# Optimization experiments

Measured on AMD Instinct MI355X. Metric: run time of the kernel, lower is better.

Reference implementation:

```python
import jax, jax.numpy as jnp
import numpy as np

DIM = 1024
N_HEADS = 16
HEAD_DIM = DIM // N_HEADS


def setup_inputs() -> dict:
    key = jax.random.key(0)
    ks = jax.random.split(key, 5)
    B, L = 2, 2048
    q = jax.random.normal(ks[0], (B, L, DIM), dtype=jnp.float32)
    # nn.Linear weights: shape [out_features, in_features], applied as x @ W.T
    scale = 1.0 / np.sqrt(DIM)
    Wq = jax.random.normal(ks[1], (DIM, DIM), dtype=jnp.float32) * scale
    Wk = jax.random.normal(ks[2], (DIM, DIM), dtype=jnp.float32) * scale
    Wv = jax.random.normal(ks[3], (DIM, DIM), dtype=jnp.float32) * scale
    Wo = jax.random.normal(ks[4], (DIM, DIM), dtype=jnp.float32) * scale
    return {"q": q, "Wq": Wq, "Wk": Wk, "Wv": Wv, "Wo": Wo}


def reference(q, Wq, Wk, Wv, Wo):
    B, L, _ = q.shape
    kv = q  # self-attention (kv=None path)
    # projections: x @ W.T, then split heads: b l (h d) -> b h l d
    def split_heads(x):
        return x.reshape(B, L, N_HEADS, HEAD_DIM).transpose(0, 2, 1, 3)
    qh = split_heads(q @ Wq.T)
    kh = split_heads(kv @ Wk.T)
    vh = split_heads(kv @ Wv.T)
    # scaled dot-product attention; scale = sqrt(head_dim)
    scores = jnp.einsum('bhid,bhjd->bhij', qh, kh) / jnp.sqrt(
        jnp.asarray(HEAD_DIM, dtype=qh.dtype))
    attn = jax.nn.softmax(scores, axis=-1)
    out = jnp.einsum('bhij,bhjd->bhid', attn, vh)
    # b h l d -> b l (h d)
    out = out.transpose(0, 2, 1, 3).reshape(B, L, DIM)
    return out @ Wo.T
```

## Files before the change

kernel.cpp:

```cpp
#include <hip/hip_runtime.h>


#define DIMN 1024
#define NH 16
#define HD 64
#define BB 2
#define LL 2048

typedef float f32x4 __attribute__((ext_vector_type(4)));
typedef short s16x8 __attribute__((ext_vector_type(8)));

#define QSCALE 0.18033688011112042f

static __device__ __forceinline__ unsigned short f2bf(float f) {
  unsigned u = __float_as_uint(f);
  u += 0x7fffu + ((u >> 16) & 1u);
  return (unsigned short)(u >> 16);
}
static __device__ __forceinline__ unsigned packbf2(float lo, float hi) {
  return (unsigned)f2bf(lo) | ((unsigned)f2bf(hi) << 16);
}
static __device__ __forceinline__ float xexp2(float x) {
#if __has_builtin(__builtin_amdgcn_exp2f)
  return __builtin_amdgcn_exp2f(x);
#else
  return exp2f(x);
#endif
}
static __device__ __forceinline__ s16x8 cvt8(float4 a, float4 b) {
  s16x8 r;
  r[0] = (short)f2bf(a.x); r[1] = (short)f2bf(a.y);
  r[2] = (short)f2bf(a.z); r[3] = (short)f2bf(a.w);
  r[4] = (short)f2bf(b.x); r[5] = (short)f2bf(b.y);
  r[6] = (short)f2bf(b.z); r[7] = (short)f2bf(b.w);
  return r;
}
static __device__ __forceinline__ void gld16(const unsigned short* g,
                                             unsigned short* l) {
#if __has_builtin(__builtin_amdgcn_global_load_lds)
  __builtin_amdgcn_global_load_lds(
      (const __attribute__((address_space(1))) void*)g,
      (__attribute__((address_space(3))) void*)l, 16, 0, 0);
#else
  ((uint4*)l)[threadIdx.x & 63] = ((const uint4*)g)[0];
#endif
}


__global__ __launch_bounds__(256) void cvt_all(
    const float* __restrict__ X, const float* __restrict__ Wq,
    const float* __restrict__ Wk, const float* __restrict__ Wv,
    const float* __restrict__ Wo, unsigned short* __restrict__ out) {
  const int blk = blockIdx.x;
  const float* src;
  unsigned short* dst;
  size_t off;
  if (blk < 2048) {
    src = X; dst = out; off = (size_t)blk * 2048;
  } else {
    int s = (blk - 2048) >> 9;
    src = (s == 0) ? Wq : (s == 1) ? Wk : (s == 2) ? Wv : Wo;
    dst = out + ((size_t)1 << 22) + (size_t)s * (1u << 20);
    off = (size_t)((blk - 2048) & 511) * 2048;
  }
  size_t i = off + (size_t)threadIdx.x * 8;
  float4 v0 = *(const float4*)(src + i);
  float4 v1 = *(const float4*)(src + i + 4);
  uint4 o;
  o.x = packbf2(v0.x, v0.y); o.y = packbf2(v0.z, v0.w);
  o.z = packbf2(v1.x, v1.y); o.w = packbf2(v1.z, v1.w);
  *(uint4*)(dst + i) = o;
}

__global__ __launch_bounds__(256) void gemm_qkv(
    const unsigned short* __restrict__ Xb, const unsigned short* __restrict__ Wb,
    unsigned short* __restrict__ Qb, unsigned short* __restrict__ Kb,
    unsigned short* __restrict__ VT) {
  __shared__ __align__(16) unsigned short Al[128 * 32];
  __shared__ __align__(16) unsigned short Bl[128 * 32];
  const int m0 = blockIdx.x * 128;
  const int n0g = blockIdx.y * 128;
  const int sel = n0g >> 10;
  const int tid = threadIdx.x;
  const int w = tid >> 6, lane = tid & 63;
  const int c = lane & 15, quad = lane >> 4;
  const int wm = (w & 1) * 64, wn = (w >> 1) * 64;

  f32x4 zero = {0.f, 0.f, 0.f, 0.f};
  f32x4 acc[4][4];
#pragma unroll
  for (int i = 0; i < 4; ++i)
#pragma unroll
    for (int j = 0; j < 4; ++j) acc[i][j] = zero;

  const int srow = w * 32 + (lane >> 2);
  const int scol = (lane & 3) * 8;
  const unsigned short* gA = Xb + (size_t)(m0 + srow) * DIMN + scol;
  const unsigned short* gB = Wb + (size_t)(n0g + srow) * DIMN + scol;
  unsigned short* lA0 = Al + (w * 32) * 32;
  unsigned short* lA1 = Al + (w * 32 + 16) * 32;
  unsigned short* lB0 = Bl + (w * 32) * 32;
  unsigned short* lB1 = Bl + (w * 32 + 16) * 32;

  for (int k0 = 0; k0 < DIMN; k0 += 32) {
    __syncthreads();
    gld16(gA + k0, lA0);
    gld16(gA + k0 + 16 * DIMN, lA1);
    gld16(gB + k0, lB0);
    gld16(gB + k0 + 16 * DIMN, lB1);
    __syncthreads();
    s16x8 a[4], b[4];
#pragma unroll
    for (int i = 0; i < 4; ++i)
      a[i] = *(const s16x8*)&Al[(wm + i * 16 + c) * 32 + quad * 8];
#pragma unroll
    for (int j = 0; j < 4; ++j)
      b[j] = *(const s16x8*)&Bl[(wn + j * 16 + c) * 32 + quad * 8];
    if (sel != 2) {
#pragma unroll
      for (int i = 0; i < 4; ++i)
#pragma unroll
        for (int j = 0; j < 4; ++j)
          acc[i][j] = __builtin_amdgcn_mfma_f32_16x16x32_bf16(a[i], b[j], acc[i][j], 0, 0, 0);
    } else {
#pragma unroll
      for (int i = 0; i < 4; ++i)
#pragma unroll
        for (int j = 0; j < 4; ++j)
          acc[i][j] = __builtin_amdgcn_mfma_f32_16x16x32_bf16(b[j], a[i], acc[i][j], 0, 0, 0);
    }
  }

  const int n0 = n0g & 1023;
  if (sel != 2) {
    unsigned short* Out = (sel == 0) ? Qb : Kb;
    const float scale = (sel == 0) ? QSCALE : 1.0f;
#pragma unroll
    for (int i = 0; i < 4; ++i)
#pragma unroll
      for (int j = 0; j < 4; ++j)
#pragma unroll
        for (int r = 0; r < 4; ++r) {
          int row = m0 + wm + i * 16 + quad * 4 + r;
          int col = n0 + wn + j * 16 + c;
          Out[(((size_t)(row >> 11) * NH + (col >> 6)) * LL + (row & 2047)) * HD + (col & 63)] =
              f2bf(acc[i][j][r] * scale);
        }
  } else {
#pragma unroll
    for (int i = 0; i < 4; ++i) {
      const int p64 = (i >> 1) * 32 + (i & 1);
#pragma unroll
      for (int j = 0; j < 4; ++j)
#pragma unroll
        for (int r = 0; r < 4; ++r) {
          int n = n0 + wn + j * 16 + quad * 4 + r;
          int m = m0 + wm + p64 + 2 * c;
          VT[(((size_t)(m >> 11) * NH + (n >> 6)) * HD + (n & 63)) * LL + (m & 2047)] =
              f2bf(acc[i][j][r]);
        }
    }
  }
}

__global__ __launch_bounds__(256) void gemm_o(
    const unsigned short* __restrict__ A, const unsigned short* __restrict__ Wob,
    float* __restrict__ Out) {
  __shared__ __align__(16) unsigned short Al[128 * 32];
  __shared__ __align__(16) unsigned short Bl[64 * 32];
  const int m0 = blockIdx.x * 128;
  const int n0 = blockIdx.y * 64;
  const int tid = threadIdx.x;
  const int w = tid >> 6, lane = tid & 63;
  const int c = lane & 15, quad = lane >> 4;
  const int wm = (w & 1) * 64, wn = (w >> 1) * 32;

  f32x4 zero = {0.f, 0.f, 0.f, 0.f};
  f32x4 acc[4][2];
#pragma unroll
  for (int i = 0; i < 4; ++i)
#pragma unroll
    for (int j = 0; j < 2; ++j) acc[i][j] = zero;

  const int srow = w * 32 + (lane >> 2);
  const int brow = w * 16 + (lane >> 2);
  const int scol = (lane & 3) * 8;
  const unsigned short* gA = A + (size_t)(m0 + srow) * DIMN + scol;
  const unsigned short* gB = Wob + (size_t)(n0 + brow) * DIMN + scol;
  unsigned short* lA0 = Al + (w * 32) * 32;
  unsigned short* lA1 = Al + (w * 32 + 16) * 32;
  unsigned short* lB0 = Bl + (w * 16) * 32;

  for (int k0 = 0; k0 < DIMN; k0 += 32) {
    __syncthreads();
    gld16(gA + k0, lA0);
    gld16(gA + k0 + 16 * DIMN, lA1);
    gld16(gB + k0, lB0);
    __syncthreads();
    s16x8 a[4], b[2];
#pragma unroll
    for (int i = 0; i < 4; ++i)
      a[i] = *(const s16x8*)&Al[(wm + i * 16 + c) * 32 + quad * 8];
#pragma unroll
    for (int j = 0; j < 2; ++j)
      b[j] = *(const s16x8*)&Bl[(wn + j * 16 + c) * 32 + quad * 8];
#pragma unroll
    for (int i = 0; i < 4; ++i)
#pragma unroll
      for (int j = 0; j < 2; ++j)
        acc[i][j] = __builtin_amdgcn_mfma_f32_16x16x32_bf16(a[i], b[j], acc[i][j], 0, 0, 0);
  }

#pragma unroll
  for (int i = 0; i < 4; ++i)
#pragma unroll
    for (int j = 0; j < 2; ++j)
#pragma unroll
      for (int r = 0; r < 4; ++r)
        Out[(size_t)(m0 + wm + i * 16 + quad * 4 + r) * DIMN + n0 + wn + j * 16 + c] =
            acc[i][j][r];
}

__global__ __launch_bounds__(256) void attn4(
    const unsigned short* __restrict__ Qb, const unsigned short* __restrict__ Kb,
    const unsigned short* __restrict__ VT, unsigned short* __restrict__ AO) {
  __shared__ __align__(16) unsigned short Kl[128 * 64];
  __shared__ __align__(16) unsigned short Vtl[64 * 128];
  __shared__ __align__(16) unsigned short Pl[4][32][72];

  const int bh = blockIdx.y;
  const int tid = threadIdx.x;
  const int w = tid >> 6, lane = tid & 63;
  const int c = lane & 15, quad = lane >> 4;
  const int q0 = blockIdx.x * 128 + w * 32;

  const unsigned short* Qh = Qb + (size_t)bh * LL * HD;
  const unsigned short* Kh = Kb + (size_t)bh * LL * HD;
  const unsigned short* Vh = VT + (size_t)bh * HD * LL;

  s16x8 qf[2][2];
#pragma unroll
  for (int m = 0; m < 2; ++m)
#pragma unroll
    for (int f = 0; f < 2; ++f)
      qf[m][f] = *(const s16x8*)(Qh + (size_t)(q0 + m * 16 + c) * HD + f * 32 + quad * 8);

  f32x4 zero = {0.f, 0.f, 0.f, 0.f};
  f32x4 o[2][4];
  float lsum[2][4];
#pragma unroll
  for (int m = 0; m < 2; ++m)
#pragma unroll
    for (int r = 0; r < 4; ++r) lsum[m][r] = 0.f;
#pragma unroll
  for (int m = 0; m < 2; ++m)
#pragma unroll
    for (int dc = 0; dc < 4; ++dc) o[m][dc] = zero;

  const int l8 = lane >> 3, p8 = lane & 7;
  const unsigned short* gK = Kh + (size_t)(w * 8 + l8) * HD + ((p8 ^ l8) * 8);
  unsigned short* lK = (unsigned short*)Kl + (w * 8) * 64;
  const int l16 = lane >> 4, p16 = lane & 15;
  const int vrow = w * 4 + l16;
  const unsigned short* gV = Vh + (size_t)vrow * LL + ((p16 ^ vrow) * 8);
  unsigned short* lV = (unsigned short*)Vtl + (w * 4) * 128;

  const int kpa = (quad ^ (c & 7)) * 8;
  const int kpb = ((quad + 4) ^ (c & 7)) * 8;

  for (int k0 = 0; k0 < LL; k0 += 128) {
    __syncthreads();
#pragma unroll
    for (int s = 0; s < 4; ++s)
      gld16(gK + (size_t)(k0 + s * 32) * HD, lK + s * 32 * 64);
#pragma unroll
    for (int s = 0; s < 4; ++s)
      gld16(gV + (size_t)(s * 16) * LL + k0, lV + s * 16 * 128);
    __syncthreads();

#pragma unroll
    for (int g = 0; g < 2; ++g) {
      f32x4 s[2][4];
#pragma unroll
      for (int t4 = 0; t4 < 4; ++t4) {
        const int t = g * 4 + t4;
        s16x8 kfa = *(const s16x8*)&Kl[(t * 16 + c) * 64 + kpa];
        s16x8 kfb = *(const s16x8*)&Kl[(t * 16 + c) * 64 + kpb];
#pragma unroll
        for (int m = 0; m < 2; ++m) {
          s[m][t4] = __builtin_amdgcn_mfma_f32_16x16x32_bf16(qf[m][0], kfa, zero, 0, 0, 0);
          s[m][t4] = __builtin_amdgcn_mfma_f32_16x16x32_bf16(qf[m][1], kfb, s[m][t4], 0, 0, 0);
        }
      }
#pragma unroll
      for (int m = 0; m < 2; ++m)
#pragma unroll
        for (int r = 0; r < 4; ++r) {
          float p0 = xexp2(s[m][0][r]);
          float p1 = xexp2(s[m][1][r]);
          float p2 = xexp2(s[m][2][r]);
          float p3 = xexp2(s[m][3][r]);
          lsum[m][r] += (p0 + p1) + (p2 + p3);
          unsigned pk01 = __builtin_amdgcn_perm(__float_as_uint(p1), __float_as_uint(p0), 0x07060302u);
          unsigned pk23 = __builtin_amdgcn_perm(__float_as_uint(p3), __float_as_uint(p2), 0x07060302u);
          int row = m * 16 + quad * 4 + r;
          *(unsigned*)&Pl[w][row][2 * c] = pk01;
          *(unsigned*)&Pl[w][row][32 + 2 * c] = pk23;
        }
      asm volatile("s_waitcnt lgkmcnt(0)" ::: "memory");

#pragma unroll
      for (int kh = 0; kh < 2; ++kh) {
        const int kk = g * 2 + kh;
        s16x8 pf0 = *(const s16x8*)&Pl[w][c][kh * 32 + quad * 8];
        s16x8 pf1 = *(const s16x8*)&Pl[w][16 + c][kh * 32 + quad * 8];
#pragma unroll
        for (int dc = 0; dc < 4; ++dc) {
          s16x8 vf = *(const s16x8*)&Vtl[(dc * 16 + c) * 128 + (((kk * 4 + quad) ^ c) * 8)];
          o[0][dc] = __builtin_amdgcn_mfma_f32_16x16x32_bf16(pf0, vf, o[0][dc], 0, 0, 0);
          o[1][dc] = __builtin_amdgcn_mfma_f32_16x16x32_bf16(pf1, vf, o[1][dc], 0, 0, 0);
        }
      }
    }
  }

  const int bi = bh >> 4, h = bh & 15;
#pragma unroll
  for (int m = 0; m < 2; ++m)
#pragma unroll
    for (int r = 0; r < 4; ++r) {
      float l = lsum[m][r];
      l += __shfl_xor(l, 1);
      l += __shfl_xor(l, 2);
      l += __shfl_xor(l, 4);
      l += __shfl_xor(l, 8);
      float inv = 1.0f / l;
      int li = q0 + m * 16 + quad * 4 + r;
#pragma unroll
      for (int dc = 0; dc < 4; ++dc)
        AO[((size_t)bi * LL + li) * DIMN + h * HD + dc * 16 + c] = f2bf(o[m][dc][r] * inv);
    }
}

__global__ __launch_bounds__(64) void qkv_proj_f(
    const float* __restrict__ X, const float* __restrict__ Wq,
    const float* __restrict__ Wk, const float* __restrict__ Wv,
    unsigned short* __restrict__ Qb, unsigned short* __restrict__ Kb,
    unsigned short* __restrict__ VT) {
  const int m0 = blockIdx.x * 64;
  const int n0g = blockIdx.y * 64;
  const int sel = n0g >> 10;
  const int n0 = n0g & 1023;
  const float* W = (sel == 0) ? Wq : (sel == 1) ? Wk : Wv;
  const int lane = threadIdx.x;
  const int c = lane & 15, quad = lane >> 4;

  f32x4 zero = {0.f, 0.f, 0.f, 0.f};
  f32x4 acc[4][4];
#pragma unroll
  for (int i = 0; i < 4; ++i)
#pragma unroll
    for (int j = 0; j < 4; ++j) acc[i][j] = zero;

  const float* ab = X + (size_t)(m0 + c) * DIMN + quad * 8;
  const float* bb = W + (size_t)(n0 + c) * DIMN + quad * 8;

  for (int k0 = 0; k0 < DIMN; k0 += 32) {
    s16x8 a[4], b[4];
#pragma unroll
    for (int i = 0; i < 4; ++i) {
      const float* p = ab + i * 16 * DIMN + k0;
      a[i] = cvt8(*(const float4*)p, *(const float4*)(p + 4));
    }
#pragma unroll
    for (int j = 0; j < 4; ++j) {
      const float* p = bb + j * 16 * DIMN + k0;
      b[j] = cvt8(*(const float4*)p, *(const float4*)(p + 4));
    }
    if (sel != 2) {
#pragma unroll
      for (int i = 0; i < 4; ++i)
#pragma unroll
        for (int j = 0; j < 4; ++j)
          acc[i][j] = __builtin_amdgcn_mfma_f32_16x16x32_bf16(a[i], b[j], acc[i][j], 0, 0, 0);
    } else {
#pragma unroll
      for (int i = 0; i < 4; ++i)
#pragma unroll
        for (int j = 0; j < 4; ++j)
          acc[i][j] = __builtin_amdgcn_mfma_f32_16x16x32_bf16(b[j], a[i], acc[i][j], 0, 0, 0);
    }
  }

  if (sel != 2) {
    unsigned short* Out = (sel == 0) ? Qb : Kb;
    const float scale = (sel == 0) ? QSCALE : 1.0f;
#pragma unroll
    for (int i = 0; i < 4; ++i)
#pragma unroll
      for (int j = 0; j < 4; ++j)
#pragma unroll
        for (int r = 0; r < 4; ++r) {
          int row = m0 + i * 16 + quad * 4 + r;
          int nl = n0 + j * 16 + c;
          int bi = row >> 11, li = row & 2047;
          int h = nl >> 6, d = nl & 63;
          Out[(((size_t)bi * NH + h) * LL + li) * HD + d] = f2bf(acc[i][j][r] * scale);
        }
  } else {
#pragma unroll
    for (int i = 0; i < 4; ++i) {
      const int p64 = (i >> 1) * 32 + (i & 1);
#pragma unroll
      for (int j = 0; j < 4; ++j)
#pragma unroll
        for (int r = 0; r < 4; ++r) {
          int n = n0 + j * 16 + quad * 4 + r;
          int l = m0 + p64 + 2 * c;
          int h = n >> 6, d = n & 63;
          int bi = l >> 11, li = l & 2047;
          VT[(((size_t)bi * NH + h) * HD + d) * LL + li] = f2bf(acc[i][j][r]);
        }
    }
  }
}

__global__ __launch_bounds__(64) void o_proj_f(
    const unsigned short* __restrict__ A, const float* __restrict__ Wo,
    float* __restrict__ Out) {
  const int m0 = blockIdx.x * 64, n0 = blockIdx.y * 64;
  const int lane = threadIdx.x;
  const int c = lane & 15, quad = lane >> 4;

  f32x4 zero = {0.f, 0.f, 0.f, 0.f};
  f32x4 acc[4][4];
#pragma unroll
  for (int i = 0; i < 4; ++i)
#pragma unroll
    for (int j = 0; j < 4; ++j) acc[i][j] = zero;

  const unsigned short* ab = A + (size_t)(m0 + c) * DIMN + quad * 8;
  const float* bb = Wo + (size_t)(n0 + c) * DIMN + quad * 8;

  for (int k0 = 0; k0 < DIMN; k0 += 32) {
    s16x8 a[4], b[4];
#pragma unroll
    for (int i = 0; i < 4; ++i) a[i] = *(const s16x8*)(ab + i * 16 * DIMN + k0);
#pragma unroll
    for (int j = 0; j < 4; ++j) {
      const float* p = bb + j * 16 * DIMN + k0;
      b[j] = cvt8(*(const float4*)p, *(const float4*)(p + 4));
    }
#pragma unroll
    for (int i = 0; i < 4; ++i)
#pragma unroll
      for (int j = 0; j < 4; ++j)
        acc[i][j] = __builtin_amdgcn_mfma_f32_16x16x32_bf16(a[i], b[j], acc[i][j], 0, 0, 0);
  }

#pragma unroll
  for (int i = 0; i < 4; ++i)
#pragma unroll
    for (int j = 0; j < 4; ++j)
#pragma unroll
      for (int r = 0; r < 4; ++r)
        Out[(size_t)(m0 + i * 16 + quad * 4 + r) * DIMN + n0 + j * 16 + c] = acc[i][j][r];
}

extern "C" void kernel_launch(void* const* d_in, const int* in_sizes, int n_in,
                              void* d_out, int out_size, void* d_ws, size_t ws_size,
                              hipStream_t stream) {
  const float* X = (const float*)d_in[0];
  const float* Wq = (const float*)d_in[1];
  const float* Wk = (const float*)d_in[2];
  const float* Wv = (const float*)d_in[3];
  const float* Wo = (const float*)d_in[4];
  float* Out = (float*)d_out;

  const size_t M1 = (size_t)1 << 20;
  unsigned short* ws16 = (unsigned short*)d_ws;

  if (ws_size >= (size_t)48 * 1024 * 1024) {
    unsigned short* Xb = ws16;
    unsigned short* Wb = ws16 + 4 * M1;
    unsigned short* Qb = ws16 + 8 * M1;
    unsigned short* Kb = ws16 + 12 * M1;
    unsigned short* VT = ws16 + 16 * M1;
    unsigned short* AO = ws16 + 20 * M1;
    cvt_all<<<4096, 256, 0, stream>>>(X, Wq, Wk, Wv, Wo, ws16);
    gemm_qkv<<<dim3(32, 24), 256, 0, stream>>>(Xb, Wb, Qb, Kb, VT);
    attn4<<<dim3(LL / 128, BB * NH), 256, 0, stream>>>(Qb, Kb, VT, AO);
    gemm_o<<<dim3(32, 16), 256, 0, stream>>>(AO, Wb + 3 * M1, Out);
  } else {
    unsigned short* Qb = ws16;
    unsigned short* Kb = ws16 + 4 * M1;
    unsigned short* VT = ws16 + 8 * M1;
    unsigned short* AO = ws16 + 12 * M1;
    qkv_proj_f<<<dim3(64, 48), 64, 0, stream>>>(X, Wq, Wk, Wv, Qb, Kb, VT);
    attn4<<<dim3(LL / 128, BB * NH), 256, 0, stream>>>(Qb, Kb, VT, AO);
    o_proj_f<<<dim3(64, 16), 64, 0, stream>>>(AO, Wo, Out);
  }
}
```

Before: 196.9 us.

## Keep softmax probabilities in registers via transposed MFMA and permuted V layout

The attention kernel now computes S^T by swapping the MFMA operands, so each lane holds the probabilities for its own query column. These are packed straight into bf16 A-operands for the PV MFMA, which removes the LDS round trip through the P buffer and its wait. To make this work, the V^T columns are written by the projection kernels in a permuted key order (vpos). K/V tiles are also double-buffered, so the next tile's loads are issued while the current one is computed, leaving one barrier per iteration. Output stores become packed 8-byte writes, and the row-sum reduction shrinks to two shuffles. The cost is double the LDS footprint, which may reduce occupancy.

```diff
diff --git a/kernel.cpp b/kernel.cpp
--- a/kernel.cpp
+++ b/kernel.cpp
@@ -46,6 +46,9 @@
 #endif
 }
 
+static __device__ __forceinline__ int vpos(int s128) {
+  return (s128 & 0x60) | ((s128 & 0x0C) << 1) | ((s128 & 0x10) >> 2) | (s128 & 3);
+}
 
 __global__ __launch_bounds__(256) void cvt_all(
     const float* __restrict__ X, const float* __restrict__ Wq,
@@ -149,16 +152,19 @@
   } else {
 #pragma unroll
     for (int i = 0; i < 4; ++i) {
-      const int p64 = (i >> 1) * 32 + (i & 1);
+      const int pos = vpos(wm + i * 16 + 2 * 0 + 0);
 #pragma unroll
       for (int j = 0; j < 4; ++j)
 #pragma unroll
         for (int r = 0; r < 4; ++r) {
           int n = n0 + wn + j * 16 + quad * 4 + r;
-          int m = m0 + wm + p64 + 2 * c;
-          VT[(((size_t)(m >> 11) * NH + (n >> 6)) * HD + (n & 63)) * LL + (m & 2047)] =
+          int sp = vpos(wm + i * 16 + c);
+          int m = m0 + sp;
+          int bi = (m0 + wm) >> 11;
+          VT[(((size_t)bi * NH + (n >> 6)) * HD + (n & 63)) * LL + (m & 2047)] =
               f2bf(acc[i][j][r]);
         }
+      (void)pos;
     }
   }
 }
@@ -221,12 +227,11 @@
             acc[i][j][r];
 }
 
-__global__ __launch_bounds__(256) void attn4(
+__global__ __launch_bounds__(256) void attn5(
     const unsigned short* __restrict__ Qb, const unsigned short* __restrict__ Kb,
     const unsigned short* __restrict__ VT, unsigned short* __restrict__ AO) {
-  __shared__ __align__(16) unsigned short Kl[128 * 64];
-  __shared__ __align__(16) unsigned short Vtl[64 * 128];
-  __shared__ __align__(16) unsigned short Pl[4][32][72];
+  __shared__ __align__(16) unsigned short Kl[2 * 128 * 64];
+  __shared__ __align__(16) unsigned short Vtl[2 * 64 * 128];
 
   const int bh = blockIdx.y;
   const int tid = threadIdx.x;
@@ -247,11 +252,7 @@
 
   f32x4 zero = {0.f, 0.f, 0.f, 0.f};
   f32x4 o[2][4];
-  float lsum[2][4];
-#pragma unroll
-  for (int m = 0; m < 2; ++m)
-#pragma unroll
-    for (int r = 0; r < 4; ++r) lsum[m][r] = 0.f;
+  float lsum[2] = {0.f, 0.f};
 #pragma unroll
   for (int m = 0; m < 2; ++m)
 #pragma unroll
@@ -259,87 +260,105 @@
 
   const int l8 = lane >> 3, p8 = lane & 7;
   const unsigned short* gK = Kh + (size_t)(w * 8 + l8) * HD + ((p8 ^ l8) * 8);
-  unsigned short* lK = (unsigned short*)Kl + (w * 8) * 64;
   const int l16 = lane >> 4, p16 = lane & 15;
   const int vrow = w * 4 + l16;
   const unsigned short* gV = Vh + (size_t)vrow * LL + ((p16 ^ vrow) * 8);
-  unsigned short* lV = (unsigned short*)Vtl + (w * 4) * 128;
 
   const int kpa = (quad ^ (c & 7)) * 8;
   const int kpb = ((quad + 4) ^ (c & 7)) * 8;
 
-  for (int k0 = 0; k0 < LL; k0 += 128) {
+#define STAGE(buf, k0)                                                        \
+  do {                                                                        \
+    unsigned short* lK_ = Kl + (buf) * (128 * 64) + (w * 8) * 64;             \
+    unsigned short* lV_ = Vtl + (buf) * (64 * 128) + (w * 4) * 128;           \
+    _Pragma("unroll")                                                         \
+    for (int s_ = 0; s_ < 4; ++s_)                                            \
+      gld16(gK + (size_t)((k0) + s_ * 32) * HD, lK_ + s_ * 32 * 64);          \
+    _Pragma("unroll")                                                         \
+    for (int s_ = 0; s_ < 4; ++s_)                                            \
+      gld16(gV + (size_t)(s_ * 16) * LL + (k0), lV_ + s_ * 16 * 128);         \
+  } while (0)
+
+  STAGE(0, 0);
+
+  for (int it = 0; it < LL / 128; ++it) {
     __syncthreads();
-#pragma unroll
-    for (int s = 0; s < 4; ++s)
-      gld16(gK + (size_t)(k0 + s * 32) * HD, lK + s * 32 * 64);
-#pragma unroll
-    for (int s = 0; s < 4; ++s)
-      gld16(gV + (size_t)(s * 16) * LL + k0, lV + s * 16 * 128);
-    __syncthreads();
+    if (it + 1 < LL / 128) STAGE((it + 1) & 1, (it + 1) * 128);
+    const unsigned short* Kt = Kl + (it & 1) * (128 * 64);
+    const unsigned short* Vt = Vtl + (it & 1) * (64 * 128);
 
 #pragma unroll
     for (int g = 0; g < 2; ++g) {
       f32x4 s[2][4];
 #pragma unroll
       for (int t4 = 0; t4 < 4; ++t4) {
-        const int t = g * 4 + t4;
-        s16x8 kfa = *(const s16x8*)&Kl[(t * 16 + c) * 64 + kpa];
-        s16x8 kfb = *(const s16x8*)&Kl[(t * 16 + c) * 64 + kpb];
+        const unsigned short* kr = Kt + ((g * 4 + t4) * 16 + c) * 64;
+        s16x8 kfa = *(const s16x8*)(kr + kpa);
+        s16x8 kfb = *(const s16x8*)(kr + kpb);
 #pragma unroll
         for (int m = 0; m < 2; ++m) {
-          s[m][t4] = __builtin_amdgcn_mfma_f32_16x16x32_bf16(qf[m][0], kfa, zero, 0, 0, 0);
-          s[m][t4] = __builtin_amdgcn_mfma_f32_16x16x32_bf16(qf[m][1], kfb, s[m][t4], 0, 0, 0);
+          s[m][t4] = __builtin_amdgcn_mfma_f32_16x16x32_bf16(kfa, qf[m][0], zero, 0, 0, 0);
+          s[m][t4] = __builtin_amdgcn_mfma_f32_16x16x32_bf16(kfb, qf[m][1], s[m][t4], 0, 0, 0);
         }
       }
-#pragma unroll
-      for (int m = 0; m < 2; ++m)
-#pragma unroll
-        for (int r = 0; r < 4; ++r) {
-          float p0 = xexp2(s[m][0][r]);
-          float p1 = xexp2(s[m][1][r]);
-          float p2 = xexp2(s[m][2][r]);
-          float p3 = xexp2(s[m][3][r]);
-          lsum[m][r] += (p0 + p1) + (p2 + p3);
-          unsigned pk01 = __builtin_amdgcn_perm(__float_as_uint(p1), __float_as_uint(p0), 0x07060302u);
-          unsigned pk23 = __builtin_amdgcn_perm(__float_as_uint(p3), __float_as_uint(p2), 0x07060302u);
-          int row = m * 16 + quad * 4 + r;
-          *(unsigned*)&Pl[w][row][2 * c] = pk01;
-          *(unsigned*)&Pl[w][row][32 + 2 * c] = pk23;
-        }
-      asm volatile("s_waitcnt lgkmcnt(0)" ::: "memory");
-
+      float p[2][4][4];
+#pragma unroll
+      for (int m = 0; m < 2; ++m) {
+        float acc_l = 0.f;
+#pragma unroll
+        for (int t4 = 0; t4 < 4; ++t4)
+#pragma unroll
+          for (int r = 0; r < 4; ++r) {
+            float e = xexp2(s[m][t4][r]);
+            p[m][t4][r] = e;
+            acc_l += e;
+          }
+        lsum[m] += acc_l;
+      }
 #pragma unroll
       for (int kh = 0; kh < 2; ++kh) {
         const int kk = g * 2 + kh;
-        s16x8 pf0 = *(const s16x8*)&Pl[w][c][kh * 32 + quad * 8];
-        s16x8 pf1 = *(const s16x8*)&Pl[w][16 + c][kh * 32 + quad * 8];
+        s16x8 pf[2];
+#pragma unroll
+        for (int m = 0; m < 2; ++m) {
+          unsigned u0 = __builtin_amdgcn_perm(__float_as_uint(p[m][2 * kh][1]),
+                                              __float_as_uint(p[m][2 * kh][0]), 0x07060302u);
+          unsigned u1 = __builtin_amdgcn_perm(__float_as_uint(p[m][2 * kh][3]),
+                                              __float_as_uint(p[m][2 * kh][2]), 0x07060302u);
+          unsigned u2 = __builtin_amdgcn_perm(__float_as_uint(p[m][2 * kh + 1][1]),
+                                              __float_as_uint(p[m][2 * kh + 1][0]), 0x07060302u);
+          unsigned u3 = __builtin_amdgcn_perm(__float_as_uint(p[m][2 * kh + 1][3]),
+                                              __float_as_uint(p[m][2 * kh + 1][2]), 0x07060302u);
+          unsigned pu[4] = {u0, u1, u2, u3};
+          pf[m] = *(const s16x8*)pu;
+        }
 #pragma unroll
         for (int dc = 0; dc < 4; ++dc) {
-          s16x8 vf = *(const s16x8*)&Vtl[(dc * 16 + c) * 128 + (((kk * 4 + quad) ^ c) * 8)];
-          o[0][dc] = __builtin_amdgcn_mfma_f32_16x16x32_bf16(pf0, vf, o[0][dc], 0, 0, 0);
-          o[1][dc] = __builtin_amdgcn_mfma_f32_16x16x32_bf16(pf1, vf, o[1][dc], 0, 0, 0);
+          s16x8 vf = *(const s16x8*)(Vt + (dc * 16 + c) * 128 + (((kk * 4 + quad) ^ c) * 8));
+          o[0][dc] = __builtin_amdgcn_mfma_f32_16x16x32_bf16(vf, pf[0], o[0][dc], 0, 0, 0);
+          o[1][dc] = __builtin_amdgcn_mfma_f32_16x16x32_bf16(vf, pf[1], o[1][dc], 0, 0, 0);
         }
       }
     }
   }
+#undef STAGE
 
   const int bi = bh >> 4, h = bh & 15;
 #pragma unroll
-  for (int m = 0; m < 2; ++m)
-#pragma unroll
-    for (int r = 0; r < 4; ++r) {
-      float l = lsum[m][r];
-      l += __shfl_xor(l, 1);
-      l += __shfl_xor(l, 2);
-      l += __shfl_xor(l, 4);
-      l += __shfl_xor(l, 8);
-      float inv = 1.0f / l;
-      int li = q0 + m * 16 + quad * 4 + r;
-#pragma unroll
-      for (int dc = 0; dc < 4; ++dc)
-        AO[((size_t)bi * LL + li) * DIMN + h * HD + dc * 16 + c] = f2bf(o[m][dc][r] * inv);
-    }
+  for (int m = 0; m < 2; ++m) {
+    float l = lsum[m];
+    l += __shfl_xor(l, 16);
+    l += __shfl_xor(l, 32);
+    float inv = 1.0f / l;
+    unsigned short* dst = AO + ((size_t)bi * LL + q0 + m * 16 + c) * DIMN + h * HD + quad * 4;
+#pragma unroll
+    for (int dc = 0; dc < 4; ++dc) {
+      uint2 st;
+      st.x = packbf2(o[m][dc][0] * inv, o[m][dc][1] * inv);
+      st.y = packbf2(o[m][dc][2] * inv, o[m][dc][3] * inv);
+      *(uint2*)(dst + dc * 16) = st;
+    }
+  }
 }
 
 __global__ __launch_bounds__(64) void qkv_proj_f(
@@ -369,13 +388,13 @@
     s16x8 a[4], b[4];
 #pragma unroll
     for (int i = 0; i < 4; ++i) {
-      const float* p = ab + i * 16 * DIMN + k0;
-      a[i] = cvt8(*(const float4*)p, *(const float4*)(p + 4));
+      const float* pp = ab + i * 16 * DIMN + k0;
+      a[i] = cvt8(*(const float4*)pp, *(const float4*)(pp + 4));
     }
 #pragma unroll
     for (int j = 0; j < 4; ++j) {
-      const float* p = bb + j * 16 * DIMN + k0;
-      b[j] = cvt8(*(const float4*)p, *(const float4*)(p + 4));
+      const float* pp = bb + j * 16 * DIMN + k0;
+      b[j] = cvt8(*(const float4*)pp, *(const float4*)(pp + 4));
     }
     if (sel != 2) {
 #pragma unroll
@@ -410,16 +429,16 @@
   } else {
 #pragma unroll
     for (int i = 0; i < 4; ++i) {
-      const int p64 = (i >> 1) * 32 + (i & 1);
 #pragma unroll
       for (int j = 0; j < 4; ++j)
 #pragma unroll
         for (int r = 0; r < 4; ++r) {
           int n = n0 + j * 16 + quad * 4 + r;
-          int l = m0 + p64 + 2 * c;
+          int s128 = (m0 & 64) + i * 16 + c;
+          int m = (m0 & ~127) + vpos(s128);
           int h = n >> 6, d = n & 63;
-          int bi = l >> 11, li = l & 2047;
-          VT[(((size_t)bi * NH + h) * HD + d) * LL + li] = f2bf(acc[i][j][r]);
+          int bi = m0 >> 11;
+          VT[(((size_t)bi * NH + h) * HD + d) * LL + (m & 2047)] = f2bf(acc[i][j][r]);
         }
     }
   }
@@ -448,8 +467,8 @@
     for (int i = 0; i < 4; ++i) a[i] = *(const s16x8*)(ab + i * 16 * DIMN + k0);
 #pragma unroll
     for (int j = 0; j < 4; ++j) {
-      const float* p = bb + j * 16 * DIMN + k0;
-      b[j] = cvt8(*(const float4*)p, *(const float4*)(p + 4));
+      const float* pp = bb + j * 16 * DIMN + k0;
+      b[j] = cvt8(*(const float4*)pp, *(const float4*)(pp + 4));
     }
 #pragma unroll
     for (int i = 0; i < 4; ++i)
@@ -489,7 +508,7 @@
     unsigned short* AO = ws16 + 20 * M1;
     cvt_all<<<4096, 256, 0, stream>>>(X, Wq, Wk, Wv, Wo, ws16);
     gemm_qkv<<<dim3(32, 24), 256, 0, stream>>>(Xb, Wb, Qb, Kb, VT);
-    attn4<<<dim3(LL / 128, BB * NH), 256, 0, stream>>>(Qb, Kb, VT, AO);
+    attn5<<<dim3(LL / 128, BB * NH), 256, 0, stream>>>(Qb, Kb, VT, AO);
     gemm_o<<<dim3(32, 16), 256, 0, stream>>>(AO, Wb + 3 * M1, Out);
   } else {
     unsigned short* Qb = ws16;
@@ -497,7 +516,7 @@
     unsigned short* VT = ws16 + 8 * M1;
     unsigned short* AO = ws16 + 12 * M1;
     qkv_proj_f<<<dim3(64, 48), 64, 0, stream>>>(X, Wq, Wk, Wv, Qb, Kb, VT);
-    attn4<<<dim3(LL / 128, BB * NH), 256, 0, stream>>>(Qb, Kb, VT, AO);
+    attn5<<<dim3(LL / 128, BB * NH), 256, 0, stream>>>(Qb, Kb, VT, AO);
     o_proj_f<<<dim3(64, 16), 64, 0, stream>>>(AO, Wo, Out);
   }
 }
```

Result: faster. 191.5 us (-2.7%).
